# Kernel tuning notes

Hardware: AMD Instinct MI355X
Metric: run time of the kernel (lower is better)

Reference implementation:

```python
import jax, jax.numpy as jnp
import numpy as np

# Complete 4-ary tree, leaves at depth 8, heap layout (children of i are 4i+1..4i+4).
B_ARY = 4
DEPTH = 8          # depths 0..8, leaves at depth 8
H = 512            # hidden_channels
IN = 512           # in_channels
OUT = 256          # out_channels
L = 2              # num_layers
LEVEL_STARTS = np.array([(B_ARY ** d - 1) // (B_ARY - 1) for d in range(DEPTH + 2)])
N = int(LEVEL_STARTS[-1])  # 87381


def setup_inputs() -> dict:
    key = jax.random.key(0)
    ks = jax.random.split(key, 12)
    x = jax.random.normal(ks[0], (N, IN), jnp.float32)

    # tree structure (numpy, deterministic)
    n_internal = int(LEVEL_STARTS[DEPTH])
    child_idx = np.zeros((N, B_ARY), np.int32)
    child_mask = np.zeros((N, B_ARY), np.int32)
    internal = np.arange(n_internal)
    child_idx[:n_internal] = (internal[:, None] * B_ARY + 1 + np.arange(B_ARY)[None, :]).astype(np.int32)
    child_mask[:n_internal] = 1
    node_parent = np.full(N, -1, np.int64)
    node_parent[1:] = (np.arange(1, N) - 1) // B_ARY
    node_depth = np.zeros(N, np.int64)
    for d in range(DEPTH + 1):
        node_depth[LEVEL_STARTS[d]:LEVEL_STARTS[d + 1]] = d
    is_leaf = node_depth == DEPTH
    edge_index = np.stack([np.arange(1, N), node_parent[1:]]).astype(np.int64)
    batch = np.zeros(N, np.int64)

    s = 0.02
    params = dict(
        W_in=jax.random.normal(ks[1], (IN, H), jnp.float32) * s,
        b_in=jnp.zeros((H,), jnp.float32),
        W_ioux=jax.random.normal(ks[2], (L, H, 3 * H), jnp.float32) * s,
        b_ioux=jnp.zeros((L, 3 * H), jnp.float32),
        W_iouh=jax.random.normal(ks[3], (L, H, 3 * H), jnp.float32) * s,
        b_iouh=jnp.zeros((L, 3 * H), jnp.float32),
        W_fx=jax.random.normal(ks[4], (L, H, H), jnp.float32) * s,
        b_fx=jnp.zeros((L, H), jnp.float32),
        W_fh=jax.random.normal(ks[5], (L, H, H), jnp.float32) * s,
        b_fh=jnp.zeros((L, H), jnp.float32),
        W_out=jax.random.normal(ks[6], (H, OUT), jnp.float32) * s,
        b_out=jnp.zeros((OUT,), jnp.float32),
    )
    return dict(
        x=x,
        edge_index=jnp.asarray(edge_index),
        batch=jnp.asarray(batch),
        node_depth=jnp.asarray(node_depth),
        node_parent=jnp.asarray(node_parent),
        is_leaf=jnp.asarray(is_leaf),
        child_idx=jnp.asarray(child_idx),
        child_mask=jnp.asarray(child_mask),
        **params,
    )


def reference(x, edge_index, batch, node_depth, node_parent, is_leaf,
              child_idx, child_mask,
              W_in, b_in, W_ioux, b_ioux, W_iouh, b_iouh,
              W_fx, b_fx, W_fh, b_fh, W_out, b_out):
    cm = child_mask.astype(x.dtype)  # [N, B]
    h = jax.nn.relu(x @ W_in + b_in)  # input projection (dropout = eval mode identity)
    for l in range(L):
        hidden = jnp.zeros((N, H), x.dtype)
        cell = jnp.zeros((N, H), x.dtype)
        # bottom-up over tree levels; levels are contiguous static slices
        for d in range(DEPTH, -1, -1):
            s, e = int(LEVEL_STARTS[d]), int(LEVEL_STARTS[d + 1])
            xl = h[s:e]                                   # [n_d, H]
            ci = child_idx[s:e]                           # [n_d, B]
            m = cm[s:e][..., None]                        # [n_d, B, 1]
            ch = hidden[ci] * m                           # masked child hidden
            cc = cell[ci] * m                             # masked child cell
            h_sum = ch.sum(axis=1)                        # child-sum
            iou = xl @ W_ioux[l] + b_ioux[l] + h_sum @ W_iouh[l] + b_iouh[l]
            i, o, u = jnp.split(iou, 3, axis=-1)
            i = jax.nn.sigmoid(i)
            o = jax.nn.sigmoid(o)
            u = jnp.tanh(u)
            f = jax.nn.sigmoid((xl @ W_fx[l] + b_fx[l])[:, None, :] + ch @ W_fh[l] + b_fh[l])
            c = i * u + (f * cc).sum(axis=1)
            hl = o * jnp.tanh(c)
            hidden = hidden.at[s:e].set(hl)
            cell = cell.at[s:e].set(c)
        h = hidden
    node_emb = h @ W_out + b_out                          # [N, OUT]
    tree_emb = jax.ops.segment_sum(node_emb, batch, num_segments=1)  # 'sum' aggregation
    return node_emb, tree_emb
```

## Files before the change

kernel.cpp:

```cpp
#include <hip/hip_runtime.h>

typedef __bf16 bf16;
typedef __bf16 bf16x8 __attribute__((ext_vector_type(8)));
typedef float f32x4 __attribute__((ext_vector_type(4)));

#define NN 87381
#define NINT 21845
#define NLEAF 65536
#define LEAF_START 21845

__device__ __forceinline__ float sigmoidf_(float x) {
    return 1.0f / (1.0f + __expf(-x));
}
__device__ __forceinline__ float tanhf_(float x) {
    return 1.0f - 2.0f / (__expf(2.0f * x) + 1.0f);
}

__device__ __forceinline__ void gload_lds16(const bf16* g, bf16* l) {
    __builtin_amdgcn_global_load_lds(
        (const __attribute__((address_space(1))) unsigned int*)g,
        (__attribute__((address_space(3))) unsigned int*)l, 16, 0, 0);
}

__device__ __forceinline__ int xcd_swz(int bid, int nwg) {
    int q = nwg >> 3, r = nwg & 7;
    int x = bid & 7, i = bid >> 3;
    return (x < r ? x * (q + 1) : r * (q + 1) + (x - r) * q) + i;
}

#define SWZ(r, kc) ((((r) << 3) | ((kc) ^ ((r) & 7))) << 3)

__global__ void tconv_kernel(const float* __restrict__ W, bf16* __restrict__ Wt,
                             int NR, int total) {
    int idx = blockIdx.x * 256 + threadIdx.x;
    if (idx >= total) return;
    int n = idx >> 9;
    int k = idx & 511;
    Wt[idx] = (bf16)W[(size_t)k * NR + n];
}

__global__ void convx_kernel(const float* __restrict__ X, bf16* __restrict__ Y, int total4) {
    int idx = blockIdx.x * 256 + threadIdx.x;
    if (idx >= total4) return;
    const float4 f = *reinterpret_cast<const float4*>(X + (size_t)idx * 4);
    bf16 o[4] = {(bf16)f.x, (bf16)f.y, (bf16)f.z, (bf16)f.w};
    *reinterpret_cast<ushort2*>(Y + (size_t)idx * 4 + 0) = *reinterpret_cast<ushort2*>(&o[0]);
    *reinterpret_cast<ushort2*>(Y + (size_t)idx * 4 + 2) = *reinterpret_cast<ushort2*>(&o[2]);
}

#define MFMA_COMPUTE_2x4(As, Bs, acc, wm, wn, lm, quad)                          \
    _Pragma("unroll")                                                            \
    for (int kk = 0; kk < 64; kk += 32) {                                        \
        const int kc_ = (kk >> 3) + quad;                                        \
        bf16x8 areg[2], breg[4];                                                 \
        _Pragma("unroll")                                                        \
        for (int mi = 0; mi < 2; ++mi)                                           \
            areg[mi] = *reinterpret_cast<const bf16x8*>(                         \
                &(As)[SWZ(wm + mi * 16 + lm, kc_)]);                             \
        _Pragma("unroll")                                                        \
        for (int ni = 0; ni < 4; ++ni)                                           \
            breg[ni] = *reinterpret_cast<const bf16x8*>(                         \
                &(Bs)[SWZ(wn + ni * 16 + lm, kc_)]);                             \
        _Pragma("unroll")                                                        \
        for (int mi = 0; mi < 2; ++mi)                                           \
            _Pragma("unroll")                                                    \
            for (int ni = 0; ni < 4; ++ni)                                       \
                acc[mi][ni] = __builtin_amdgcn_mfma_f32_16x16x32_bf16(           \
                    areg[mi], breg[ni], acc[mi][ni], 0, 0, 0);                   \
    }

__global__ __launch_bounds__(512)
void gemm_kernel(const bf16* __restrict__ A, const bf16* __restrict__ Bt,
                 int bstride, int K, int ntiles,
                 float* __restrict__ Cf, bf16* __restrict__ Cb,
                 const float* __restrict__ bias1, const float* __restrict__ bias2,
                 int M, int N, int relu, int swz)
{
    __shared__ __align__(16) bf16 As[2][128 * 64];
    __shared__ __align__(16) bf16 Bs[2][128 * 64];
    const int tid  = threadIdx.x;
    const int wave = tid >> 6;
    const int lane = tid & 63;
    int bid = blockIdx.x;
    if (swz) bid = xcd_swz(bid, (int)gridDim.x);
    const int bm = (bid / ntiles) * 128;
    const int bn = (bid % ntiles) * 128;
    const int wm = (wave & 3) * 32;
    const int wn = (wave >> 2) * 64;
    const int lm   = lane & 15;
    const int quad = lane >> 4;

    f32x4 acc[2][4];
#pragma unroll
    for (int i = 0; i < 2; ++i)
#pragma unroll
        for (int j = 0; j < 4; ++j) acc[i][j] = (f32x4){0.f, 0.f, 0.f, 0.f};

    const bf16* aptr[2];
    const bf16* bptr[2];
    int loff[2];
#pragma unroll
    for (int i = 0; i < 2; ++i) {
        int c   = i * 512 + tid;
        int r   = c >> 3;
        int kc8 = ((c & 7) ^ (r & 7)) << 3;
        int gr  = bm + r; gr = (gr < M) ? gr : (M - 1);
        aptr[i] = A + (size_t)gr * K + kc8;
        bptr[i] = Bt + (size_t)(bn + r) * bstride + kc8;
        loff[i] = c << 3;
    }

    auto stage = [&](int buf, int t) {
        const int kofs = t << 6;
#pragma unroll
        for (int i = 0; i < 2; ++i)
            gload_lds16(aptr[i] + kofs, &As[0][0] + buf * (128 * 64) + loff[i]);
#pragma unroll
        for (int i = 0; i < 2; ++i)
            gload_lds16(bptr[i] + kofs, &Bs[0][0] + buf * (128 * 64) + loff[i]);
    };

    const int nk = K >> 6;
    stage(0, 0);
    __syncthreads();
    int cur = 0;
    for (int t = 0; t < nk; ++t) {
        if (t + 1 < nk) stage(cur ^ 1, t + 1);
        MFMA_COMPUTE_2x4(As[cur], Bs[cur], acc, wm, wn, lm, quad);
        __syncthreads();
        cur ^= 1;
    }

#pragma unroll
    for (int ni = 0; ni < 4; ++ni) {
        int col = bn + wn + ni * 16 + lm;
        float bsum = (bias1 ? bias1[col] : 0.f) + (bias2 ? bias2[col] : 0.f);
#pragma unroll
        for (int mi = 0; mi < 2; ++mi) {
#pragma unroll
            for (int r = 0; r < 4; ++r) {
                int row = bm + wm + mi * 16 + quad * 4 + r;
                if (row < M) {
                    float v = acc[mi][ni][r] + bsum;
                    if (relu) v = (v > 0.f) ? v : 0.f;
                    if (Cf) Cf[(size_t)row * N + col] = v;
                    else    Cb[(size_t)row * N + col] = (bf16)v;
                }
            }
        }
    }
}

__global__ __launch_bounds__(512)
void iou_fused_kernel(const bf16* __restrict__ A, const bf16* __restrict__ wiou,
                      const float* __restrict__ bx1, const float* __restrict__ bx2,
                      const float* __restrict__ fcs, const bf16* __restrict__ xout,
                      bf16* __restrict__ hout, bf16* __restrict__ cellout,
                      bf16* __restrict__ hsout,
                      int M, int swz)
{
    __shared__ __align__(16) bf16 As[2][128 * 64];
    __shared__ __align__(16) bf16 Bs[2][3 * 64 * 64];
    const int tid  = threadIdx.x;
    const int wave = tid >> 6;
    const int lane = tid & 63;
    int bid = blockIdx.x;
    if (swz) bid = xcd_swz(bid, (int)gridDim.x);
    const int bm = (bid >> 3) * 128;
    const int bn = (bid & 7) * 64;
    if (bm >= M) return;
    const int wm   = (wave & 3) * 32;
    const int wn   = (wave >> 2) * 32;
    const int lm   = lane & 15;
    const int quad = lane >> 4;

    f32x4 acc[3][2][2];
#pragma unroll
    for (int g = 0; g < 3; ++g)
#pragma unroll
        for (int i = 0; i < 2; ++i)
#pragma unroll
            for (int j = 0; j < 2; ++j) acc[g][i][j] = (f32x4){0.f, 0.f, 0.f, 0.f};

    const bf16* aptr[2];
    int aoff[2];
#pragma unroll
    for (int i = 0; i < 2; ++i) {
        int c   = i * 512 + tid;
        int r   = c >> 3;
        int kc8 = ((c & 7) ^ (r & 7)) << 3;
        int gr  = bm + r; gr = (gr < M) ? gr : (M - 1);
        aptr[i] = A + ((size_t)gr << 9) + kc8;
        aoff[i] = c << 3;
    }
    const bf16* bptr[3];
    int boff[3];
#pragma unroll
    for (int i = 0; i < 3; ++i) {
        int c   = i * 512 + tid;
        int g   = c >> 9;
        int cg  = c & 511;
        int r   = cg >> 3;
        int kc8 = ((cg & 7) ^ (r & 7)) << 3;
        bptr[i] = wiou + (size_t)(g * 512 + bn + r) * 512 + kc8;
        boff[i] = c << 3;
    }

    auto stage = [&](int buf, int t) {
        const int kofs = t << 6;
#pragma unroll
        for (int i = 0; i < 2; ++i)
            gload_lds16(aptr[i] + kofs, &As[0][0] + buf * (128 * 64) + aoff[i]);
#pragma unroll
        for (int i = 0; i < 3; ++i)
            gload_lds16(bptr[i] + kofs, &Bs[0][0] + buf * (3 * 64 * 64) + boff[i]);
    };

    stage(0, 0);
    __syncthreads();
    int cur = 0;
    for (int t = 0; t < 8; ++t) {
        if (t + 1 < 8) stage(cur ^ 1, t + 1);
#pragma unroll
        for (int kk = 0; kk < 64; kk += 32) {
            const int kc_ = (kk >> 3) + quad;
            bf16x8 areg[2];
#pragma unroll
            for (int mi = 0; mi < 2; ++mi)
                areg[mi] = *reinterpret_cast<const bf16x8*>(
                    &As[cur][SWZ(wm + mi * 16 + lm, kc_)]);
            bf16x8 breg[3][2];
#pragma unroll
            for (int g = 0; g < 3; ++g)
#pragma unroll
                for (int ni = 0; ni < 2; ++ni)
                    breg[g][ni] = *reinterpret_cast<const bf16x8*>(
                        &Bs[cur][g * 4096 + SWZ(wn + ni * 16 + lm, kc_)]);
#pragma unroll
            for (int g = 0; g < 3; ++g)
#pragma unroll
                for (int mi = 0; mi < 2; ++mi)
#pragma unroll
                    for (int ni = 0; ni < 2; ++ni)
                        acc[g][mi][ni] = __builtin_amdgcn_mfma_f32_16x16x32_bf16(
                            areg[mi], breg[g][ni], acc[g][mi][ni], 0, 0, 0);
        }
        __syncthreads();
        cur ^= 1;
    }

#pragma unroll
    for (int ni = 0; ni < 2; ++ni) {
        int col = bn + wn + ni * 16 + lm;
        float bi = bx1[col]        + bx2[col];
        float bo = bx1[col + 512]  + bx2[col + 512];
        float bu = bx1[col + 1024] + bx2[col + 1024];
#pragma unroll
        for (int mi = 0; mi < 2; ++mi) {
            int rbase = bm + wm + mi * 16 + quad * 4;
            float hsum = 0.f;
#pragma unroll
            for (int r = 0; r < 4; ++r) {
                int row = rbase + r;
                if (row < M) {
                    float ax = 0.f, aox = 0.f, aux = 0.f;
                    if (xout) {
                        ax  = (float)xout[(size_t)row * 2048 + col];
                        aox = (float)xout[(size_t)row * 2048 + 512 + col];
                        aux = (float)xout[(size_t)row * 2048 + 1024 + col];
                    }
                    float i_ = sigmoidf_(acc[0][mi][ni][r] + ax + bi);
                    float o_ = sigmoidf_(acc[1][mi][ni][r] + aox + bo);
                    float u_ = tanhf_(acc[2][mi][ni][r] + aux + bu);
                    float c  = i_ * u_ + (fcs ? fcs[(size_t)row * 512 + col] : 0.f);
                    bf16 hb  = (bf16)(o_ * tanhf_(c));
                    cellout[(size_t)row * 512 + col] = (bf16)c;
                    hout[(size_t)row * 512 + col] = hb;
                    hsum += (float)hb;
                }
            }
            if (hsout && rbase < M)
                hsout[(size_t)(rbase >> 2) * 512 + col] = (bf16)hsum;
        }
    }
}

__global__ __launch_bounds__(512)
void cf_kernel(const bf16* __restrict__ hc, const bf16* __restrict__ cellc,
               const bf16* __restrict__ wfh, const bf16* __restrict__ xout,
               const float* __restrict__ bf1, const float* __restrict__ bf2,
               float* __restrict__ fcs, int E, int swz)
{
    const int M = 4 * E;
    __shared__ __align__(16) bf16 As[2][128 * 64];
    __shared__ __align__(16) bf16 Bs[2][128 * 64];
    const int tid  = threadIdx.x;
    const int wave = tid >> 6;
    const int lane = tid & 63;
    int bid = blockIdx.x;
    if (swz) bid = xcd_swz(bid, (int)gridDim.x);
    const int bm = (bid >> 2) * 128;
    const int bn = (bid & 3) * 128;
    if (bm >= M) return;
    const int wm   = (wave & 3) * 32;
    const int wn   = (wave >> 2) * 64;
    const int lm   = lane & 15;
    const int quad = lane >> 4;

    f32x4 acc[2][4];
#pragma unroll
    for (int i = 0; i < 2; ++i)
#pragma unroll
        for (int j = 0; j < 4; ++j) acc[i][j] = (f32x4){0.f, 0.f, 0.f, 0.f};

    const bf16* aptr[2];
    const bf16* bptr[2];
    int loff[2];
#pragma unroll
    for (int i = 0; i < 2; ++i) {
        int c   = i * 512 + tid;
        int r   = c >> 3;
        int kc8 = ((c & 7) ^ (r & 7)) << 3;
        int gr  = bm + r; gr = (gr < M) ? gr : (M - 1);
        aptr[i] = hc + ((size_t)gr << 9) + kc8;
        bptr[i] = wfh + (size_t)(bn + r) * 512 + kc8;
        loff[i] = c << 3;
    }

    auto stage = [&](int buf, int t) {
        const int kofs = t << 6;
#pragma unroll
        for (int i = 0; i < 2; ++i)
            gload_lds16(aptr[i] + kofs, &As[0][0] + buf * (128 * 64) + loff[i]);
#pragma unroll
        for (int i = 0; i < 2; ++i)
            gload_lds16(bptr[i] + kofs, &Bs[0][0] + buf * (128 * 64) + loff[i]);
    };

    stage(0, 0);
    __syncthreads();
    int cur = 0;
    for (int t = 0; t < 8; ++t) {
        if (t + 1 < 8) stage(cur ^ 1, t + 1);
        MFMA_COMPUTE_2x4(As[cur], Bs[cur], acc, wm, wn, lm, quad);
        __syncthreads();
        cur ^= 1;
    }

#pragma unroll
    for (int ni = 0; ni < 4; ++ni) {
        int col = bn + wn + ni * 16 + lm;
        float bsum = bf1[col] + bf2[col];
#pragma unroll
        for (int mi = 0; mi < 2; ++mi) {
            int R0 = bm + wm + mi * 16;
            if (R0 + quad * 4 < M) {
                int p = (R0 >> 2) + quad;
                float pf = (float)xout[(size_t)p * 2048 + 1536 + col] + bsum;
                float fc = 0.f;
#pragma unroll
                for (int r = 0; r < 4; ++r) {
                    int row = R0 + quad * 4 + r;
                    fc += sigmoidf_(acc[mi][ni][r] + pf) *
                          (float)cellc[(size_t)row * 512 + col];
                }
                fcs[(size_t)p * 512 + col] = fc;
            }
        }
    }
}

#define R1_BLOCKS 2048
#define R1_ROWS 43
__global__ void reduce1_kernel(const float* __restrict__ ne, float* __restrict__ partial)
{
    int t = threadIdx.x;
    int b = blockIdx.x;
    int r0 = b * R1_ROWS;
    int r1 = r0 + R1_ROWS; r1 = (r1 < NN) ? r1 : NN;
    float acc = 0.f;
    for (int r = r0; r < r1; ++r) acc += ne[(size_t)r * 256 + t];
    partial[(size_t)b * 256 + t] = acc;
}
__global__ void reduce2_kernel(const float* __restrict__ partial, float* __restrict__ partial2)
{
    int t = threadIdx.x;
    int b = blockIdx.x;
    float acc = 0.f;
    for (int i = 0; i < 32; ++i) acc += partial[(size_t)(b * 32 + i) * 256 + t];
    partial2[(size_t)b * 256 + t] = acc;
}
__global__ void reduce3_kernel(const float* __restrict__ partial2, float* __restrict__ tree)
{
    int t = threadIdx.x;
    float acc = 0.f;
    for (int i = 0; i < 64; ++i) acc += partial2[(size_t)i * 256 + t];
    tree[t] = acc;
}

extern "C" void kernel_launch(void* const* d_in, const int* in_sizes, int n_in,
                              void* d_out, int out_size, void* d_ws, size_t ws_size,
                              hipStream_t stream)
{
    const float* x      = (const float*)d_in[0];
    const float* W_in   = (const float*)d_in[8];
    const float* b_in   = (const float*)d_in[9];
    const float* W_ioux = (const float*)d_in[10];
    const float* b_ioux = (const float*)d_in[11];
    const float* W_iouh = (const float*)d_in[12];
    const float* b_iouh = (const float*)d_in[13];
    const float* W_fx   = (const float*)d_in[14];
    const float* b_fx   = (const float*)d_in[15];
    const float* W_fh   = (const float*)d_in[16];
    const float* b_fh   = (const float*)d_in[17];
    const float* W_out  = (const float*)d_in[18];
    const float* b_out  = (const float*)d_in[19];

    static const int LS[10] = {0, 1, 5, 21, 85, 341, 1365, 5461, 21845, 87381};

    char* ws = (char*)d_ws;
    size_t off = 0;
    auto take = [&](size_t bytes) -> void* {
        void* p = ws + off;
        off += (bytes + 255) & ~(size_t)255;
        return p;
    };
    bf16*  wt_in      = (bf16*) take((size_t)512 * 512 * 2);
    bf16*  wt_out     = (bf16*) take((size_t)256 * 512 * 2);
    bf16*  wt_xcat    = (bf16*) take((size_t)2 * 2048 * 512 * 2);
    bf16*  wt_iouh    = (bf16*) take((size_t)2 * 1536 * 512 * 2);
    bf16*  wt_fh      = (bf16*) take((size_t)2 * 512 * 512 * 2);
    bf16*  h          = (bf16*) take((size_t)NN * 512 * 2);
    bf16*  hint1      = (bf16*) take((size_t)NINT * 512 * 2);
    bf16*  hB         = (bf16*) take((size_t)NLEAF * 512 * 2);
    bf16*  cell_int   = (bf16*) take((size_t)NINT * 512 * 2);
    bf16*  cell_leaf  = (bf16*) take((size_t)NLEAF * 512 * 2);
    float* fcsum      = (float*)take((size_t)16384 * 512 * 4);
    bf16*  hsA        = (bf16*) take((size_t)16384 * 512 * 2);
    bf16*  hsB        = (bf16*) take((size_t)4096 * 512 * 2);
    bf16*  XOUT       = (bf16*) take((size_t)NINT * 2048 * 2);
    float* partial    = (float*)take((size_t)R1_BLOCKS * 256 * 4);
    float* partial2   = (float*)take((size_t)64 * 256 * 4);
    bf16*  xbf        = cell_int;

    dim3 blk(256), blk512(512);
    auto tgrid = [](int total) { return dim3((unsigned)((total + 255) / 256)); };

    tconv_kernel<<<tgrid(512 * 512), blk, 0, stream>>>(W_in, wt_in, 512, 512 * 512);
    tconv_kernel<<<tgrid(256 * 512), blk, 0, stream>>>(W_out, wt_out, 256, 256 * 512);
    for (int l = 0; l < 2; ++l) {
        bf16* xc = wt_xcat + (size_t)l * 2048 * 512;
        tconv_kernel<<<tgrid(1536 * 512), blk, 0, stream>>>(
            W_ioux + (size_t)l * 512 * 1536, xc, 1536, 1536 * 512);
        tconv_kernel<<<tgrid(512 * 512), blk, 0, stream>>>(
            W_fx + (size_t)l * 512 * 512, xc + (size_t)1536 * 512, 512, 512 * 512);
        tconv_kernel<<<tgrid(1536 * 512), blk, 0, stream>>>(
            W_iouh + (size_t)l * 512 * 1536, wt_iouh + (size_t)l * 1536 * 512,
            1536, 1536 * 512);
        tconv_kernel<<<tgrid(512 * 512), blk, 0, stream>>>(
            W_fh + (size_t)l * 512 * 512, wt_fh + (size_t)l * 512 * 512,
            512, 512 * 512);
    }

    auto gemm = [&](const bf16* A, const bf16* Bt, int bstride, int K,
                    float* Cf, bf16* Cb, const float* b1, const float* b2,
                    int M, int N, int relu, int swz) {
        int mt = (M + 127) / 128, nt = N / 128;
        gemm_kernel<<<dim3((unsigned)(mt * nt)), blk512, 0, stream>>>(
            A, Bt, bstride, K, nt, Cf, Cb, b1, b2, M, N, relu, swz);
    };

    convx_kernel<<<tgrid(NN * 128), blk, 0, stream>>>(x, xbf, NN * 128);
    gemm(xbf, wt_in, 512, 512, nullptr, h, b_in, nullptr, NN, 512, 1, 1);

    for (int l = 0; l < 2; ++l) {
        const bf16* wxc  = wt_xcat + (size_t)l * 2048 * 512;
        const bf16* wih  = wt_iouh + (size_t)l * 1536 * 512;
        const bf16* wfh  = wt_fh + (size_t)l * 512 * 512;
        const float* bx1 = b_ioux + (size_t)l * 1536;
        const float* bx2 = b_iouh + (size_t)l * 1536;
        const float* bf1 = b_fx + (size_t)l * 512;
        const float* bf2 = b_fh + (size_t)l * 512;

        const bf16* lin   = (l == 0) ? (h + (size_t)LEAF_START * 512) : hB;
        bf16*       lout  = (l == 0) ? hB : (h + (size_t)LEAF_START * 512);
        const bf16* hprev = (l == 0) ? h : hint1;
        bf16*       hcur  = (l == 0) ? hint1 : h;

        gemm(hprev, wxc, 512, 512, nullptr, XOUT, nullptr, nullptr,
             NINT, 2048, 0, 1);

        {
            int mt = NLEAF / 128;
            iou_fused_kernel<<<dim3((unsigned)(mt * 8)), blk512, 0, stream>>>(
                lin, wxc , bx1, bx2,
                nullptr, nullptr, lout, cell_leaf, hsA, NLEAF, 1);
        }

        for (int d = 7; d >= 0; --d) {
            int s  = LS[d];
            int E  = LS[d + 1] - LS[d];
            int cs = LS[d + 1];
            const bf16* hc = (d == 7) ? lout : (hcur + (size_t)cs * 512);
            const bf16* cc = (d == 7) ? cell_leaf : (cell_int + (size_t)cs * 512);
            bf16* hs_read  = (d & 1) ? hsA : hsB;
            bf16* hs_write = (d == 0) ? nullptr : ((d & 1) ? hsB : hsA);
            const bf16* xo = XOUT + (size_t)s * 2048;

            int mt_cf = (4 * E + 127) / 128;
            cf_kernel<<<dim3((unsigned)(mt_cf * 4)), blk512, 0, stream>>>(
                hc, cc, wfh, xo, bf1, bf2, fcsum, E, 1);

            int mt_iou = (E + 127) / 128;
            iou_fused_kernel<<<dim3((unsigned)(mt_iou * 8)), blk512, 0, stream>>>(
                hs_read, wih, bx1, bx2, fcsum, xo,
                hcur + (size_t)s * 512, cell_int + (size_t)s * 512, hs_write, E, 1);
        }
    }

    float* node_emb = (float*)d_out;
    gemm(h, wt_out, 512, 512, node_emb, nullptr, b_out, nullptr, NN, 256, 0, 1);
    reduce1_kernel<<<dim3(R1_BLOCKS), blk, 0, stream>>>(node_emb, partial);
    reduce2_kernel<<<dim3(64), blk, 0, stream>>>(partial, partial2);
    reduce3_kernel<<<dim3(1), blk, 0, stream>>>(partial2, node_emb + (size_t)NN * 256);
}
```

Measured before the change: 1.720 ms.

## Fuse forget-gate and IOU kernels into one per-level kernel

Measured after the change: 1.831 ms. +6.5%, slower.

```diff
diff --git a/kernel.cpp b/kernel.cpp
--- a/kernel.cpp
+++ b/kernel.cpp
@@ -152,12 +152,10 @@
 }
 
 __global__ __launch_bounds__(512)
-void iou_fused_kernel(const bf16* __restrict__ A, const bf16* __restrict__ wiou,
-                      const float* __restrict__ bx1, const float* __restrict__ bx2,
-                      const float* __restrict__ fcs, const bf16* __restrict__ xout,
-                      bf16* __restrict__ hout, bf16* __restrict__ cellout,
-                      bf16* __restrict__ hsout,
-                      int M, int swz)
+void leaf_kernel(const bf16* __restrict__ A, const bf16* __restrict__ wiou,
+                 const float* __restrict__ bx1, const float* __restrict__ bx2,
+                 bf16* __restrict__ hout, bf16* __restrict__ cellout,
+                 bf16* __restrict__ hsout, int M, int swz)
 {
     __shared__ __align__(16) bf16 As[2][128 * 64];
     __shared__ __align__(16) bf16 Bs[2][3 * 64 * 64];
@@ -263,16 +261,10 @@
             for (int r = 0; r < 4; ++r) {
                 int row = rbase + r;
                 if (row < M) {
-                    float ax = 0.f, aox = 0.f, aux = 0.f;
-                    if (xout) {
-                        ax  = (float)xout[(size_t)row * 2048 + col];
-                        aox = (float)xout[(size_t)row * 2048 + 512 + col];
-                        aux = (float)xout[(size_t)row * 2048 + 1024 + col];
-                    }
-                    float i_ = sigmoidf_(acc[0][mi][ni][r] + ax + bi);
-                    float o_ = sigmoidf_(acc[1][mi][ni][r] + aox + bo);
-                    float u_ = tanhf_(acc[2][mi][ni][r] + aux + bu);
-                    float c  = i_ * u_ + (fcs ? fcs[(size_t)row * 512 + col] : 0.f);
+                    float i_ = sigmoidf_(acc[0][mi][ni][r] + bi);
+                    float o_ = sigmoidf_(acc[1][mi][ni][r] + bo);
+                    float u_ = tanhf_(acc[2][mi][ni][r] + bu);
+                    float c  = i_ * u_;
                     bf16 hb  = (bf16)(o_ * tanhf_(c));
                     cellout[(size_t)row * 512 + col] = (bf16)c;
                     hout[(size_t)row * 512 + col] = hb;
@@ -286,55 +278,158 @@
 }
 
 __global__ __launch_bounds__(512)
-void cf_kernel(const bf16* __restrict__ hc, const bf16* __restrict__ cellc,
-               const bf16* __restrict__ wfh, const bf16* __restrict__ xout,
-               const float* __restrict__ bf1, const float* __restrict__ bf2,
-               float* __restrict__ fcs, int E, int swz)
+void level_kernel(const bf16* __restrict__ hs, const bf16* __restrict__ hc,
+                  const bf16* __restrict__ cellc,
+                  const bf16* __restrict__ wih, const bf16* __restrict__ wfh,
+                  const bf16* __restrict__ xout,
+                  const float* __restrict__ bx1, const float* __restrict__ bx2,
+                  const float* __restrict__ bf1, const float* __restrict__ bf2,
+                  float* __restrict__ fcsum,
+                  bf16* __restrict__ hout, bf16* __restrict__ cellout,
+                  bf16* __restrict__ hsout, int E, int swz)
 {
-    const int M = 4 * E;
     __shared__ __align__(16) bf16 As[2][128 * 64];
-    __shared__ __align__(16) bf16 Bs[2][128 * 64];
+    __shared__ __align__(16) bf16 Bs[2][3 * 64 * 64];
     const int tid  = threadIdx.x;
     const int wave = tid >> 6;
     const int lane = tid & 63;
     int bid = blockIdx.x;
     if (swz) bid = xcd_swz(bid, (int)gridDim.x);
-    const int bm = (bid >> 2) * 128;
-    const int bn = (bid & 3) * 128;
-    if (bm >= M) return;
-    const int wm   = (wave & 3) * 32;
-    const int wn   = (wave >> 2) * 64;
+    const int bm = (bid >> 3) * 128;
+    const int bn = (bid & 7);
+    if (bm >= E) return;
     const int lm   = lane & 15;
     const int quad = lane >> 4;
-
-    f32x4 acc[2][4];
-#pragma unroll
-    for (int i = 0; i < 2; ++i)
-#pragma unroll
-        for (int j = 0; j < 4; ++j) acc[i][j] = (f32x4){0.f, 0.f, 0.f, 0.f};
+    const int M4   = 4 * E;
+
+    {
+        const int wmA = (wave & 3) * 32;
+        const int wnA = (wave >> 2) * 32;
+        const int rb  = tid >> 3;
+        const int kcb = ((tid & 7) ^ (rb & 7)) << 3;
+        const bf16* bfp = wfh + (size_t)(bn * 64 + rb) * 512 + kcb;
+        const int  bofs = tid << 3;
+
+        for (int s = 0; s < 4; ++s) {
+            const bf16* aptrA[2]; int aoffA[2];
+#pragma unroll
+            for (int i = 0; i < 2; ++i) {
+                int c   = i * 512 + tid;
+                int r   = c >> 3;
+                int kc8 = ((c & 7) ^ (r & 7)) << 3;
+                int gr  = 4 * bm + 128 * s + r; gr = (gr < M4) ? gr : (M4 - 1);
+                aptrA[i] = hc + ((size_t)gr << 9) + kc8;
+                aoffA[i] = c << 3;
+            }
+            f32x4 accA[2][2];
+#pragma unroll
+            for (int i = 0; i < 2; ++i)
+#pragma unroll
+                for (int j = 0; j < 2; ++j) accA[i][j] = (f32x4){0.f, 0.f, 0.f, 0.f};
+
+            auto stageA = [&](int buf, int t) {
+                const int kofs = t << 6;
+#pragma unroll
+                for (int i = 0; i < 2; ++i)
+                    gload_lds16(aptrA[i] + kofs, &As[0][0] + buf * (128 * 64) + aoffA[i]);
+                gload_lds16(bfp + kofs, &Bs[0][0] + buf * (3 * 64 * 64) + bofs);
+            };
+
+            stageA(0, 0);
+            __syncthreads();
+            int cur = 0;
+            for (int t = 0; t < 8; ++t) {
+                if (t + 1 < 8) stageA(cur ^ 1, t + 1);
+#pragma unroll
+                for (int kk = 0; kk < 64; kk += 32) {
+                    const int kc_ = (kk >> 3) + quad;
+                    bf16x8 ar[2], br[2];
+#pragma unroll
+                    for (int mi = 0; mi < 2; ++mi)
+                        ar[mi] = *reinterpret_cast<const bf16x8*>(
+                            &As[cur][SWZ(wmA + mi * 16 + lm, kc_)]);
+#pragma unroll
+                    for (int ni = 0; ni < 2; ++ni)
+                        br[ni] = *reinterpret_cast<const bf16x8*>(
+                            &Bs[cur][SWZ(wnA + ni * 16 + lm, kc_)]);
+#pragma unroll
+                    for (int mi = 0; mi < 2; ++mi)
+#pragma unroll
+                        for (int ni = 0; ni < 2; ++ni)
+                            accA[mi][ni] = __builtin_amdgcn_mfma_f32_16x16x32_bf16(
+                                ar[mi], br[ni], accA[mi][ni], 0, 0, 0);
+                }
+                __syncthreads();
+                cur ^= 1;
+            }
+#pragma unroll
+            for (int ni = 0; ni < 2; ++ni) {
+                int col = bn * 64 + wnA + ni * 16 + lm;
+                float bsum = bf1[col] + bf2[col];
+#pragma unroll
+                for (int mi = 0; mi < 2; ++mi) {
+                    int lr = 128 * s + wmA + mi * 16 + quad * 4;
+                    int p  = bm + (lr >> 2);
+                    if (p < E) {
+                        float pf = (float)xout[(size_t)p * 2048 + 1536 + col] + bsum;
+                        float fc = 0.f;
+#pragma unroll
+                        for (int r = 0; r < 4; ++r) {
+                            int cr = 4 * bm + lr + r;
+                            fc += sigmoidf_(accA[mi][ni][r] + pf) *
+                                  (float)cellc[(size_t)cr * 512 + col];
+                        }
+                        fcsum[(size_t)p * 512 + col] = fc;
+                    }
+                }
+            }
+        }
+    }
+
+    const int wm = (wave & 3) * 32;
+    const int wn = (wave >> 2) * 32;
+    const int bncol = bn * 64;
+
+    f32x4 acc[3][2][2];
+#pragma unroll
+    for (int g = 0; g < 3; ++g)
+#pragma unroll
+        for (int i = 0; i < 2; ++i)
+#pragma unroll
+            for (int j = 0; j < 2; ++j) acc[g][i][j] = (f32x4){0.f, 0.f, 0.f, 0.f};
 
     const bf16* aptr[2];
-    const bf16* bptr[2];
-    int loff[2];
+    int aoff[2];
 #pragma unroll
     for (int i = 0; i < 2; ++i) {
         int c   = i * 512 + tid;
         int r   = c >> 3;
         int kc8 = ((c & 7) ^ (r & 7)) << 3;
-        int gr  = bm + r; gr = (gr < M) ? gr : (M - 1);
-        aptr[i] = hc + ((size_t)gr << 9) + kc8;
-        bptr[i] = wfh + (size_t)(bn + r) * 512 + kc8;
-        loff[i] = c << 3;
+        int gr  = bm + r; gr = (gr < E) ? gr : (E - 1);
+        aptr[i] = hs + ((size_t)gr << 9) + kc8;
+        aoff[i] = c << 3;
+    }
+    const bf16* bptr[3];
+    int boff[3];
+#pragma unroll
+    for (int i = 0; i < 3; ++i) {
+        int c   = i * 512 + tid;
+        int g   = c >> 9;
+        int cg  = c & 511;
+        int r   = cg >> 3;
+        int kc8 = ((cg & 7) ^ (r & 7)) << 3;
+        bptr[i] = wih + (size_t)(g * 512 + bncol + r) * 512 + kc8;
+        boff[i] = c << 3;
     }
 
     auto stage = [&](int buf, int t) {
         const int kofs = t << 6;
 #pragma unroll
         for (int i = 0; i < 2; ++i)
-            gload_lds16(aptr[i] + kofs, &As[0][0] + buf * (128 * 64) + loff[i]);
-#pragma unroll
-        for (int i = 0; i < 2; ++i)
-            gload_lds16(bptr[i] + kofs, &Bs[0][0] + buf * (128 * 64) + loff[i]);
+            gload_lds16(aptr[i] + kofs, &As[0][0] + buf * (128 * 64) + aoff[i]);
+#pragma unroll
+        for (int i = 0; i < 3; ++i)
+            gload_lds16(bptr[i] + kofs, &Bs[0][0] + buf * (3 * 64 * 64) + boff[i]);
     };
 
     stage(0, 0);
@@ -342,30 +437,63 @@
     int cur = 0;
     for (int t = 0; t < 8; ++t) {
         if (t + 1 < 8) stage(cur ^ 1, t + 1);
-        MFMA_COMPUTE_2x4(As[cur], Bs[cur], acc, wm, wn, lm, quad);
+#pragma unroll
+        for (int kk = 0; kk < 64; kk += 32) {
+            const int kc_ = (kk >> 3) + quad;
+            bf16x8 areg[2];
+#pragma unroll
+            for (int mi = 0; mi < 2; ++mi)
+                areg[mi] = *reinterpret_cast<const bf16x8*>(
+                    &As[cur][SWZ(wm + mi * 16 + lm, kc_)]);
+            bf16x8 breg[3][2];
+#pragma unroll
+            for (int g = 0; g < 3; ++g)
+#pragma unroll
+                for (int ni = 0; ni < 2; ++ni)
+                    breg[g][ni] = *reinterpret_cast<const bf16x8*>(
+                        &Bs[cur][g * 4096 + SWZ(wn + ni * 16 + lm, kc_)]);
+#pragma unroll
+            for (int g = 0; g < 3; ++g)
+#pragma unroll
+                for (int mi = 0; mi < 2; ++mi)
+#pragma unroll
+                    for (int ni = 0; ni < 2; ++ni)
+                        acc[g][mi][ni] = __builtin_amdgcn_mfma_f32_16x16x32_bf16(
+                            areg[mi], breg[g][ni], acc[g][mi][ni], 0, 0, 0);
+        }
         __syncthreads();
         cur ^= 1;
     }
 
 #pragma unroll
-    for (int ni = 0; ni < 4; ++ni) {
-        int col = bn + wn + ni * 16 + lm;
-        float bsum = bf1[col] + bf2[col];
+    for (int ni = 0; ni < 2; ++ni) {
+        int col = bncol + wn + ni * 16 + lm;
+        float bi = bx1[col]        + bx2[col];
+        float bo = bx1[col + 512]  + bx2[col + 512];
+        float bu = bx1[col + 1024] + bx2[col + 1024];
 #pragma unroll
         for (int mi = 0; mi < 2; ++mi) {
-            int R0 = bm + wm + mi * 16;
-            if (R0 + quad * 4 < M) {
-                int p = (R0 >> 2) + quad;
-                float pf = (float)xout[(size_t)p * 2048 + 1536 + col] + bsum;
-                float fc = 0.f;
-#pragma unroll
-                for (int r = 0; r < 4; ++r) {
-                    int row = R0 + quad * 4 + r;
-                    fc += sigmoidf_(acc[mi][ni][r] + pf) *
-                          (float)cellc[(size_t)row * 512 + col];
+            int rbase = bm + wm + mi * 16 + quad * 4;
+            float hsum = 0.f;
+#pragma unroll
+            for (int r = 0; r < 4; ++r) {
+                int row = rbase + r;
+                if (row < E) {
+                    float ax  = (float)xout[(size_t)row * 2048 + col];
+                    float aox = (float)xout[(size_t)row * 2048 + 512 + col];
+                    float aux = (float)xout[(size_t)row * 2048 + 1024 + col];
+                    float i_ = sigmoidf_(acc[0][mi][ni][r] + ax + bi);
+                    float o_ = sigmoidf_(acc[1][mi][ni][r] + aox + bo);
+                    float u_ = tanhf_(acc[2][mi][ni][r] + aux + bu);
+                    float c  = i_ * u_ + fcsum[(size_t)row * 512 + col];
+                    bf16 hb  = (bf16)(o_ * tanhf_(c));
+                    cellout[(size_t)row * 512 + col] = (bf16)c;
+                    hout[(size_t)row * 512 + col] = hb;
+                    hsum += (float)hb;
                 }
-                fcs[(size_t)p * 512 + col] = fc;
             }
+            if (hsout && rbase < E)
+                hsout[(size_t)(rbase >> 2) * 512 + col] = (bf16)hsum;
         }
     }
 }
@@ -492,9 +620,9 @@
 
         {
             int mt = NLEAF / 128;
-            iou_fused_kernel<<<dim3((unsigned)(mt * 8)), blk512, 0, stream>>>(
+            leaf_kernel<<<dim3((unsigned)(mt * 8)), blk512, 0, stream>>>(
                 lin, wxc , bx1, bx2,
-                nullptr, nullptr, lout, cell_leaf, hsA, NLEAF, 1);
+                lout, cell_leaf, hsA, NLEAF, 1);
         }
 
         for (int d = 7; d >= 0; --d) {
@@ -507,13 +635,9 @@
             bf16* hs_write = (d == 0) ? nullptr : ((d & 1) ? hsB : hsA);
             const bf16* xo = XOUT + (size_t)s * 2048;
 
-            int mt_cf = (4 * E + 127) / 128;
-            cf_kernel<<<dim3((unsigned)(mt_cf * 4)), blk512, 0, stream>>>(
-                hc, cc, wfh, xo, bf1, bf2, fcsum, E, 1);
-
-            int mt_iou = (E + 127) / 128;
-            iou_fused_kernel<<<dim3((unsigned)(mt_iou * 8)), blk512, 0, stream>>>(
-                hs_read, wih, bx1, bx2, fcsum, xo,
+            int mt = (E + 127) / 128;
+            level_kernel<<<dim3((unsigned)(mt * 8)), blk512, 0, stream>>>(
+                hs_read, hc, cc, wih, wfh, xo, bx1, bx2, bf1, bf2, fcsum,
                 hcur + (size_t)s * 512, cell_int + (size_t)s * 512, hs_write, E, 1);
         }
     }
```
